# Performance work log

Hardware: AMD Instinct MI355X
Metric: run time of the kernel (lower is better)

## Reference

```python
import jax, jax.numpy as jnp
import numpy as np

D_IN = 1024
D_OUT = 1024


def setup_inputs() -> dict:
    key = jax.random.key(0)
    kx, kq, kk, kv = jax.random.split(key, 4)
    B, S = 4, 2048
    scale = 1.0 / np.sqrt(D_IN)
    return {
        "x": jax.random.normal(kx, (B, S, D_IN), dtype=jnp.float32),
        "Wq": jax.random.normal(kq, (D_IN, D_OUT), dtype=jnp.float32) * scale,
        "Wk": jax.random.normal(kk, (D_IN, D_OUT), dtype=jnp.float32) * scale,
        "Wv": jax.random.normal(kv, (D_IN, D_OUT), dtype=jnp.float32) * scale,
    }


def reference(x, Wq, Wk, Wv):
    # x: [B, S, D_in]; single-head causal attention (dropout=0 -> identity)
    q = jnp.einsum("bsd,de->bse", x, Wq)
    k = jnp.einsum("bsd,de->bse", x, Wk)
    v = jnp.einsum("bsd,de->bse", x, Wv)
    S = x.shape[1]
    d_k = k.shape[-1]
    scores = jnp.einsum("bqe,bke->bqk", q, k) / jnp.sqrt(jnp.float32(d_k))
    causal = jnp.tril(jnp.ones((S, S), dtype=bool))  # True = keep
    scores = jnp.where(causal, scores, -jnp.inf)
    weights = jax.nn.softmax(scores, axis=-1)
    return jnp.einsum("bqk,bke->bqe", weights, v)
```

## Files before the change

kernel.cpp:

```cpp
#include <hip/hip_runtime.h>

typedef unsigned short u16;
typedef __bf16 bf16x8_v __attribute__((ext_vector_type(8)));
typedef float f32x4 __attribute__((ext_vector_type(4)));

__device__ __forceinline__ u16 f2bf(float f) {
    unsigned u = __float_as_uint(f);
    unsigned r = u + 0x7fffu + ((u >> 16) & 1u);
    return (u16)(r >> 16);
}
__device__ __forceinline__ float bf2f(u16 h) {
    return __uint_as_float(((unsigned)h) << 16);
}

__device__ __forceinline__ void gll16(const u16* g, u16* l) {
    __builtin_amdgcn_global_load_lds(
        (const __attribute__((address_space(1))) void*)g,
        (__attribute__((address_space(3))) void*)l, 16, 0, 0);
}

#define EXP_SHIFT 12.0f

__device__ __forceinline__ float* srow_ptr(u16* Sb, int b, int i) {
    return (float*)((char*)Sb + (size_t)b * 8388608 +
                    ((i >> 9) << 12) + 2048 + ((size_t)(i & 511) << 2));
}

__global__ __launch_bounds__(256) void k_prep(const float* __restrict__ x,
                                              const float* __restrict__ Wq,
                                              const float* __restrict__ Wk,
                                              const float* __restrict__ Wv,
                                              u16* __restrict__ xb,
                                              u16* __restrict__ Wt3,
                                              u16* __restrict__ Sb) {
    __shared__ float tile[32][33];
    const int bid = blockIdx.x, tid = threadIdx.x;
    if (bid < 4096) {
        int i = (bid * 256 + tid) * 8;
        float4 a = *(const float4*)(x + i);
        float4 bb = *(const float4*)(x + i + 4);
        union { int4 p; u16 h[8]; } o;
        o.h[0] = f2bf(a.x);  o.h[1] = f2bf(a.y);  o.h[2] = f2bf(a.z);  o.h[3] = f2bf(a.w);
        o.h[4] = f2bf(bb.x); o.h[5] = f2bf(bb.y); o.h[6] = f2bf(bb.z); o.h[7] = f2bf(bb.w);
        *(int4*)(xb + i) = o.p;
    } else if (bid < 7168) {
        const int w = bid - 4096;
        const int z = w >> 10, rem = w & 1023;
        const int bx = rem & 31, by = rem >> 5;
        const float* W = (z == 0) ? Wq : (z == 1) ? Wk : Wv;
        u16* Wt = Wt3 + (size_t)z * 1024 * 1024;
        const int tx = tid & 31, ty = tid >> 5;
#pragma unroll
        for (int r = 0; r < 4; ++r)
            tile[ty + r * 8][tx] = W[(by * 32 + ty + r * 8) * 1024 + bx * 32 + tx];
        __syncthreads();
#pragma unroll
        for (int r = 0; r < 4; ++r)
            Wt[(bx * 32 + ty + r * 8) * 1024 + by * 32 + tx] =
                f2bf(tile[tx][ty + r * 8]);
    } else {
        const int chunk = tid >> 7;
        const int t = tid & 127;
#pragma unroll
        for (int c = 0; c < 8; ++c) {
            const int cc = c * 2 + chunk;
            char* p = (char*)Sb + (size_t)(cc >> 2) * 8388608 +
                      ((cc & 3) << 12) + 2048;
            int4 z4 = {0, 0, 0, 0};
            *(int4*)(p + t * 16) = z4;
        }
    }
}

__device__ __forceinline__ void gemm_core_nt(const u16* __restrict__ A,
                                             const u16* __restrict__ B,
                                             int lda, int ldb, int kLen,
                                             u16* smem, f32x4 acc[4][4]) {
    u16* As = smem;
    u16* Bs = smem + 128 * 64;
    const int tid = threadIdx.x;
    const int wave = tid >> 6;
    const int lane = tid & 63;
    const int rowA = tid >> 3;
    const int kcs  = (tid & 7) ^ (rowA & 7);
    const int row16 = lane & 15;
    const int quad = lane >> 4;
    const int sw = row16 & 7;
    const int wm = (wave >> 1) * 64;
    const int wn = (wave & 1) * 64;

#pragma unroll
    for (int i = 0; i < 4; ++i)
#pragma unroll
        for (int j = 0; j < 4; ++j) {
            f32x4 z = {0.f, 0.f, 0.f, 0.f};
            acc[i][j] = z;
        }

    const u16* Ag[4]; const u16* Bg[4];
    u16 *AsB[4], *BsB[4];
#pragma unroll
    for (int u = 0; u < 4; ++u) {
        Ag[u] = A + (size_t)(u * 32 + rowA) * lda + kcs * 8;
        Bg[u] = B + (size_t)(u * 32 + rowA) * ldb + kcs * 8;
        AsB[u] = As + (u * 256 + wave * 64) * 8;
        BsB[u] = Bs + (u * 256 + wave * 64) * 8;
    }

    const int ktiles = kLen >> 6;
    for (int kt = 0; kt < ktiles; ++kt) {
        __syncthreads();
#pragma unroll
        for (int u = 0; u < 4; ++u) gll16(Ag[u] + kt * 64, AsB[u]);
#pragma unroll
        for (int u = 0; u < 4; ++u) gll16(Bg[u] + kt * 64, BsB[u]);
        __syncthreads();
#pragma unroll
        for (int h = 0; h < 2; ++h) {
            bf16x8_v af[4], bfv[4];
            const int cp = (h * 4 + quad);
#pragma unroll
            for (int i = 0; i < 4; ++i)
                af[i] = *(const bf16x8_v*)(As + (wm + i * 16 + row16) * 64 +
                                           (cp ^ sw) * 8);
#pragma unroll
            for (int j = 0; j < 4; ++j)
                bfv[j] = *(const bf16x8_v*)(Bs + (wn + j * 16 + row16) * 64 +
                                            (cp ^ sw) * 8);
#pragma unroll
            for (int i = 0; i < 4; ++i)
#pragma unroll
                for (int j = 0; j < 4; ++j)
                    acc[i][j] = __builtin_amdgcn_mfma_f32_16x16x32_bf16(
                        af[i], bfv[j], acc[i][j], 0, 0, 0);
        }
    }
}

__device__ __forceinline__ void epi_bf16(const f32x4 acc[4][4], u16* smem,
                                         u16* __restrict__ g, int ldg) {
    const int tid = threadIdx.x;
    const int wave = tid >> 6, lane = tid & 63;
    const int row16 = lane & 15, quad = lane >> 4;
    u16* Ts = smem + wave * 2048;
#pragma unroll
    for (int jh = 0; jh < 2; ++jh) {
#pragma unroll
        for (int i = 0; i < 4; ++i)
#pragma unroll
            for (int jj = 0; jj < 2; ++jj) {
                const int j = jh * 2 + jj;
#pragma unroll
                for (int r = 0; r < 4; ++r)
                    Ts[(i * 16 + quad * 4 + r) * 32 + jj * 16 + row16] =
                        f2bf(acc[i][j][r]);
            }
#pragma unroll
        for (int s = 0; s < 4; ++s) {
            const int row = s * 16 + (lane >> 2);
            int4 val = *(const int4*)(Ts + row * 32 + (lane & 3) * 8);
            *(int4*)(g + (size_t)row * ldg + jh * 32 + (lane & 3) * 8) = val;
        }
    }
}

__device__ __forceinline__ void epi_vt(const f32x4 acc[4][4], u16* smem,
                                       u16* __restrict__ Vt, int m0w, int n0w) {
    const int tid = threadIdx.x;
    const int wave = tid >> 6, lane = tid & 63;
    const int row16 = lane & 15, quad = lane >> 4;
    const int b = m0w >> 11;
    const int sBase = m0w & 2047;
    u16* Ts = smem + wave * 4608;
#pragma unroll
    for (int p = 0; p < 2; ++p) {
#pragma unroll
        for (int i = 0; i < 4; ++i)
#pragma unroll
            for (int jj = 0; jj < 2; ++jj) {
                const int j = p * 2 + jj;
                union { unsigned long long d; u16 h[4]; } o;
#pragma unroll
                for (int r = 0; r < 4; ++r) o.h[r] = f2bf(acc[i][j][r]);
                *(unsigned long long*)(Ts + (jj * 16 + row16) * 72 +
                                       i * 16 + quad * 4) = o.d;
            }
#pragma unroll
        for (int rr = 0; rr < 4; ++rr) {
            const int ln = rr * 8 + (lane >> 3);
            const int ck = lane & 7;
            int4 val = *(const int4*)(Ts + ln * 72 + ck * 8);
            const int n = n0w + p * 32 + ln;
            *(int4*)(Vt + ((size_t)b * 1024 + n) * 2048 + sBase + ck * 8) = val;
        }
    }
}

__global__ __launch_bounds__(256, 3) void k_gemm_proj(const u16* __restrict__ X,
                                                      const u16* __restrict__ Wt3,
                                                      u16* __restrict__ Qb,
                                                      u16* __restrict__ Kb,
                                                      u16* __restrict__ Vt) {
    __shared__ u16 smem[18432];
    const int n0g = blockIdx.x * 128, m0 = blockIdx.y * 128;
    f32x4 acc[4][4];
    gemm_core_nt(X + (size_t)m0 * 1024, Wt3 + (size_t)n0g * 1024, 1024, 1024, 1024,
                 smem, acc);
    const int tid = threadIdx.x, wave = tid >> 6;
    const int wm = (wave >> 1) * 64, wn = (wave & 1) * 64;
    __syncthreads();
    if (n0g < 2048) {
        u16* Y = (n0g < 1024) ? Qb : Kb;
        const int n0 = n0g & 1023;
        epi_bf16(acc, smem, Y + (size_t)(m0 + wm) * 1024 + n0 + wn, 1024);
    } else {
        epi_vt(acc, smem, Vt, m0 + wm, (n0g - 2048) + wn);
    }
}

__global__ __launch_bounds__(256, 4) void k_gemm_scores(const u16* __restrict__ Q,
                                                        const u16* __restrict__ Kb,
                                                        u16* __restrict__ Sb) {
    __shared__ u16 smem[16384];
    int t = blockIdx.x, b = blockIdx.y;
    int mt = 0;
    while ((mt + 1) * (mt + 2) / 2 <= t) ++mt;
    int nt = t - mt * (mt + 1) / 2;
    const u16* Qp = Q + (size_t)b * 2048 * 1024 + (size_t)mt * 128 * 1024;
    const u16* Kp = Kb + (size_t)b * 2048 * 1024 + (size_t)nt * 128 * 1024;
    u16* Sp = Sb + (size_t)b * 2048 * 2048;
    f32x4 acc[4][4];
    gemm_core_nt(Qp, Kp, 1024, 1024, 1024, smem, acc);
    const int tid = threadIdx.x, wave = tid >> 6, lane = tid & 63;
    const int wm = (wave >> 1) * 64, wn = (wave & 1) * 64;
    const int row16 = lane & 15, quad = lane >> 4;
    const int mBase = mt * 128 + wm;
    const int nBase = nt * 128 + wn;
    u16* Ts = smem + wave * 2048;
    float rs[4][4];
#pragma unroll
    for (int i = 0; i < 4; ++i)
#pragma unroll
        for (int r = 0; r < 4; ++r) rs[i][r] = 0.f;

    __syncthreads();
#pragma unroll
    for (int jh = 0; jh < 2; ++jh) {
#pragma unroll
        for (int i = 0; i < 4; ++i)
#pragma unroll
            for (int jj = 0; jj < 2; ++jj) {
                const int j = jh * 2 + jj;
                const int n = nBase + jh * 32 + jj * 16 + row16;
#pragma unroll
                for (int r = 0; r < 4; ++r) {
                    const int m = mBase + i * 16 + quad * 4 + r;
                    float e = 0.f;
                    if (n <= m)
                        e = __expf(acc[i][j][r] * 0.03125f - EXP_SHIFT);
                    rs[i][r] += e;
                    Ts[(i * 16 + quad * 4 + r) * 32 + jj * 16 + row16] = f2bf(e);
                }
            }
#pragma unroll
        for (int s = 0; s < 4; ++s) {
            const int row = s * 16 + (lane >> 2);
            int4 val = *(const int4*)(Ts + row * 32 + (lane & 3) * 8);
            *(int4*)(Sp + (size_t)(mBase + row) * 2048 +
                     nBase + jh * 32 + (lane & 3) * 8) = val;
        }
    }
#pragma unroll
    for (int i = 0; i < 4; ++i)
#pragma unroll
        for (int r = 0; r < 4; ++r) {
            float s = rs[i][r];
#pragma unroll
            for (int off = 1; off < 16; off <<= 1) s += __shfl_xor(s, off);
            if (row16 == 0)
                atomicAdd(srow_ptr((u16*)Sb, b, mBase + i * 16 + quad * 4 + r), s);
        }
}

__global__ __launch_bounds__(256, 4) void k_gemm_pv(u16* __restrict__ P,
                                                    const u16* __restrict__ Vt,
                                                    float* __restrict__ O) {
    __shared__ u16 smem[16384];
    const int nt = blockIdx.x, mt = 15 - blockIdx.y, b = blockIdx.z;
    const u16* Pp = P + (size_t)b * 2048 * 2048 + (size_t)mt * 128 * 2048;
    const u16* Vp = Vt + (size_t)b * 1024 * 2048 + (size_t)nt * 128 * 2048;
    f32x4 acc[4][4];
    gemm_core_nt(Pp, Vp, 2048, 2048, (mt + 1) * 128, smem, acc);
    float* Op = O + (size_t)b * 2048 * 1024;
    const int tid = threadIdx.x, wave = tid >> 6, lane = tid & 63;
    const int wm = (wave >> 1) * 64, wn = (wave & 1) * 64;
    const int row16 = lane & 15, quad = lane >> 4;
    float inv[4][4];
#pragma unroll
    for (int i = 0; i < 4; ++i)
#pragma unroll
        for (int r = 0; r < 4; ++r)
            inv[i][r] = 1.0f / *srow_ptr(P, b, mt * 128 + wm + i * 16 + quad * 4 + r);
#pragma unroll
    for (int i = 0; i < 4; ++i)
#pragma unroll
        for (int j = 0; j < 4; ++j) {
            int m = mt * 128 + wm + i * 16 + quad * 4;
            int n = nt * 128 + wn + j * 16 + row16;
#pragma unroll
            for (int r = 0; r < 4; ++r)
                Op[(size_t)(m + r) * 1024 + n] = acc[i][j][r] * inv[i][r];
        }
}

extern "C" void kernel_launch(void* const* d_in, const int* in_sizes, int n_in,
                              void* d_out, int out_size, void* d_ws, size_t ws_size,
                              hipStream_t stream) {
    const float* x  = (const float*)d_in[0];
    const float* Wq = (const float*)d_in[1];
    const float* Wk = (const float*)d_in[2];
    const float* Wv = (const float*)d_in[3];
    float* out = (float*)d_out;
    char* ws = (char*)d_ws;

    u16* xb  = (u16*)(ws);
    u16* Wt3 = (u16*)(ws + (16u << 20));
    u16* Qb  = (u16*)(ws + (22u << 20));
    u16* Kb  = (u16*)(ws + (38u << 20));
    u16* Vt  = (u16*)(ws + (54u << 20));
    u16* Sb  = (u16*)(ws + (70u << 20));

    k_prep<<<7169, 256, 0, stream>>>(x, Wq, Wk, Wv, xb, Wt3, Sb);
    k_gemm_proj<<<dim3(24, 64), 256, 0, stream>>>(xb, Wt3, Qb, Kb, Vt);
    k_gemm_scores<<<dim3(136, 4), 256, 0, stream>>>(Qb, Kb, Sb);
    k_gemm_pv<<<dim3(8, 16, 4), 256, 0, stream>>>(Sb, Vt, out);
}
```

Baseline: 232.0 us.

## Overlap V projection with scores GEMM and split-K long PV row tiles

V projection moves out of the projection kernel into a combined kernel that also runs the causal QK^T score tiles, so the score work no longer waits on the V GEMM and the two kinds of work share one launch. The scores block order is permuted across batches. The PV GEMM's longer row tiles (mt>=8) are split into two K halves that accumulate into the output with atomic adds, and the output is pre-zeroed in the prep kernel. This targets load imbalance from the triangular K lengths, at the cost of extra atomic traffic and an extra zeroing pass over the output.

```diff
diff --git a/kernel.cpp b/kernel.cpp
--- a/kernel.cpp
+++ b/kernel.cpp
@@ -32,7 +32,8 @@
                                               const float* __restrict__ Wv,
                                               u16* __restrict__ xb,
                                               u16* __restrict__ Wt3,
-                                              u16* __restrict__ Sb) {
+                                              u16* __restrict__ Sb,
+                                              float* __restrict__ O) {
     __shared__ float tile[32][33];
     const int bid = blockIdx.x, tid = threadIdx.x;
     if (bid < 4096) {
@@ -58,17 +59,23 @@
         for (int r = 0; r < 4; ++r)
             Wt[(bx * 32 + ty + r * 8) * 1024 + by * 32 + tx] =
                 f2bf(tile[tx][ty + r * 8]);
-    } else {
+    } else if (bid == 7168) {
         const int chunk = tid >> 7;
         const int t = tid & 127;
+        int4 z4 = {0, 0, 0, 0};
 #pragma unroll
         for (int c = 0; c < 8; ++c) {
             const int cc = c * 2 + chunk;
             char* p = (char*)Sb + (size_t)(cc >> 2) * 8388608 +
                       ((cc & 3) << 12) + 2048;
-            int4 z4 = {0, 0, 0, 0};
             *(int4*)(p + t * 16) = z4;
         }
+    } else {
+        float4* O4 = (float4*)O;
+        const size_t base = (size_t)(bid - 7169) * 1024 + tid;
+        float4 z4 = {0.f, 0.f, 0.f, 0.f};
+        O4[base] = z4; O4[base + 256] = z4;
+        O4[base + 512] = z4; O4[base + 768] = z4;
     }
 }
 
@@ -196,12 +203,11 @@
     }
 }
 
-__global__ __launch_bounds__(256, 3) void k_gemm_proj(const u16* __restrict__ X,
-                                                      const u16* __restrict__ Wt3,
-                                                      u16* __restrict__ Qb,
-                                                      u16* __restrict__ Kb,
-                                                      u16* __restrict__ Vt) {
-    __shared__ u16 smem[18432];
+__global__ __launch_bounds__(256, 3) void k_projqk(const u16* __restrict__ X,
+                                                   const u16* __restrict__ Wt3,
+                                                   u16* __restrict__ Qb,
+                                                   u16* __restrict__ Kb) {
+    __shared__ u16 smem[16384];
     const int n0g = blockIdx.x * 128, m0 = blockIdx.y * 128;
     f32x4 acc[4][4];
     gemm_core_nt(X + (size_t)m0 * 1024, Wt3 + (size_t)n0g * 1024, 1024, 1024, 1024,
@@ -209,20 +215,36 @@
     const int tid = threadIdx.x, wave = tid >> 6;
     const int wm = (wave >> 1) * 64, wn = (wave & 1) * 64;
     __syncthreads();
-    if (n0g < 2048) {
-        u16* Y = (n0g < 1024) ? Qb : Kb;
-        const int n0 = n0g & 1023;
-        epi_bf16(acc, smem, Y + (size_t)(m0 + wm) * 1024 + n0 + wn, 1024);
-    } else {
-        epi_vt(acc, smem, Vt, m0 + wm, (n0g - 2048) + wn);
-    }
-}
-
-__global__ __launch_bounds__(256, 4) void k_gemm_scores(const u16* __restrict__ Q,
-                                                        const u16* __restrict__ Kb,
-                                                        u16* __restrict__ Sb) {
-    __shared__ u16 smem[16384];
-    int t = blockIdx.x, b = blockIdx.y;
+    u16* Y = (n0g < 1024) ? Qb : Kb;
+    const int n0 = n0g & 1023;
+    epi_bf16(acc, smem, Y + (size_t)(m0 + wm) * 1024 + n0 + wn, 1024);
+}
+
+__global__ __launch_bounds__(256, 3) void k_mix(const u16* __restrict__ X,
+                                                const u16* __restrict__ Wt3,
+                                                u16* __restrict__ Vt,
+                                                const u16* __restrict__ Q,
+                                                const u16* __restrict__ Kb,
+                                                u16* __restrict__ Sb) {
+    __shared__ u16 smem[18432];
+    const int bid = blockIdx.x, tid = threadIdx.x;
+    const int wave = tid >> 6, lane = tid & 63;
+    const int wm = (wave >> 1) * 64, wn = (wave & 1) * 64;
+    const int row16 = lane & 15, quad = lane >> 4;
+
+    if (bid < 512) {
+        const int nv = bid & 7, m0 = (bid >> 3) * 128;
+        f32x4 acc[4][4];
+        gemm_core_nt(X + (size_t)m0 * 1024,
+                     Wt3 + (size_t)(2048 + nv * 128) * 1024, 1024, 1024, 1024,
+                     smem, acc);
+        __syncthreads();
+        epi_vt(acc, smem, Vt, m0 + wm, nv * 128 + wn);
+        return;
+    }
+    const int lin = bid - 512;
+    const int lin2 = (lin & 7) * 68 + (lin >> 3);
+    int t = lin2 % 136, b = lin2 / 136;
     int mt = 0;
     while ((mt + 1) * (mt + 2) / 2 <= t) ++mt;
     int nt = t - mt * (mt + 1) / 2;
@@ -231,9 +253,6 @@
     u16* Sp = Sb + (size_t)b * 2048 * 2048;
     f32x4 acc[4][4];
     gemm_core_nt(Qp, Kp, 1024, 1024, 1024, smem, acc);
-    const int tid = threadIdx.x, wave = tid >> 6, lane = tid & 63;
-    const int wm = (wave >> 1) * 64, wn = (wave & 1) * 64;
-    const int row16 = lane & 15, quad = lane >> 4;
     const int mBase = mt * 128 + wm;
     const int nBase = nt * 128 + wn;
     u16* Ts = smem + wave * 2048;
@@ -286,11 +305,24 @@
                                                     const u16* __restrict__ Vt,
                                                     float* __restrict__ O) {
     __shared__ u16 smem[16384];
-    const int nt = blockIdx.x, mt = 15 - blockIdx.y, b = blockIdx.z;
-    const u16* Pp = P + (size_t)b * 2048 * 2048 + (size_t)mt * 128 * 2048;
-    const u16* Vp = Vt + (size_t)b * 1024 * 2048 + (size_t)nt * 128 * 2048;
+    const int bid = blockIdx.x;
+    const int c = bid & 7, j = bid >> 3;
+    int mt, b, nt, k0, kLen;
+    bool split;
+    if (j < 32) {
+        mt = c; b = j >> 3; nt = j & 7;
+        k0 = 0; kLen = (mt + 1) * 128; split = false;
+    } else {
+        const int q = j - 32;
+        mt = 15 - c; b = q >> 4;
+        const int r = q & 15;
+        nt = r >> 1; kLen = (mt + 1) * 64; k0 = (r & 1) * kLen;
+        split = true;
+    }
+    const u16* Pp = P + (size_t)b * 2048 * 2048 + (size_t)mt * 128 * 2048 + k0;
+    const u16* Vp = Vt + (size_t)b * 1024 * 2048 + (size_t)nt * 128 * 2048 + k0;
     f32x4 acc[4][4];
-    gemm_core_nt(Pp, Vp, 2048, 2048, (mt + 1) * 128, smem, acc);
+    gemm_core_nt(Pp, Vp, 2048, 2048, kLen, smem, acc);
     float* Op = O + (size_t)b * 2048 * 1024;
     const int tid = threadIdx.x, wave = tid >> 6, lane = tid & 63;
     const int wm = (wave >> 1) * 64, wn = (wave & 1) * 64;
@@ -301,16 +333,30 @@
 #pragma unroll
         for (int r = 0; r < 4; ++r)
             inv[i][r] = 1.0f / *srow_ptr(P, b, mt * 128 + wm + i * 16 + quad * 4 + r);
-#pragma unroll
-    for (int i = 0; i < 4; ++i)
-#pragma unroll
-        for (int j = 0; j < 4; ++j) {
-            int m = mt * 128 + wm + i * 16 + quad * 4;
-            int n = nt * 128 + wn + j * 16 + row16;
-#pragma unroll
-            for (int r = 0; r < 4; ++r)
-                Op[(size_t)(m + r) * 1024 + n] = acc[i][j][r] * inv[i][r];
-        }
+    if (split) {
+#pragma unroll
+        for (int i = 0; i < 4; ++i)
+#pragma unroll
+            for (int j2 = 0; j2 < 4; ++j2) {
+                int m = mt * 128 + wm + i * 16 + quad * 4;
+                int n = nt * 128 + wn + j2 * 16 + row16;
+#pragma unroll
+                for (int r = 0; r < 4; ++r)
+                    unsafeAtomicAdd(&Op[(size_t)(m + r) * 1024 + n],
+                                    acc[i][j2][r] * inv[i][r]);
+            }
+    } else {
+#pragma unroll
+        for (int i = 0; i < 4; ++i)
+#pragma unroll
+            for (int j2 = 0; j2 < 4; ++j2) {
+                int m = mt * 128 + wm + i * 16 + quad * 4;
+                int n = nt * 128 + wn + j2 * 16 + row16;
+#pragma unroll
+                for (int r = 0; r < 4; ++r)
+                    Op[(size_t)(m + r) * 1024 + n] = acc[i][j2][r] * inv[i][r];
+            }
+    }
 }
 
 extern "C" void kernel_launch(void* const* d_in, const int* in_sizes, int n_in,
@@ -330,8 +376,8 @@
     u16* Vt  = (u16*)(ws + (54u << 20));
     u16* Sb  = (u16*)(ws + (70u << 20));
 
-    k_prep<<<7169, 256, 0, stream>>>(x, Wq, Wk, Wv, xb, Wt3, Sb);
-    k_gemm_proj<<<dim3(24, 64), 256, 0, stream>>>(xb, Wt3, Qb, Kb, Vt);
-    k_gemm_scores<<<dim3(136, 4), 256, 0, stream>>>(Qb, Kb, Sb);
-    k_gemm_pv<<<dim3(8, 16, 4), 256, 0, stream>>>(Sb, Vt, out);
-}
+    k_prep<<<9217, 256, 0, stream>>>(x, Wq, Wk, Wv, xb, Wt3, Sb, out);
+    k_projqk<<<dim3(16, 64), 256, 0, stream>>>(xb, Wt3, Qb, Kb);
+    k_mix<<<1056, 256, 0, stream>>>(xb, Wt3, Vt, Qb, Kb, Sb);
+    k_gemm_pv<<<768, 256, 0, stream>>>(Sb, Vt, out);
+}
```

Result: no change. 230.4 us (-0.7%).
